# Kernel optimization log

Measured on AMD Instinct MI355X. Metric: run time of the kernel, lower is better.

Reference implementation:

```python
import jax, jax.numpy as jnp
import numpy as np

ALPHA = 0.2
NEG = -9e15
EPS = 1e-5


def _gat(h, adj, W, a, out_features):
    # h: [B,N,Fin], adj: [B,N,N], W: [Fin,Fout], a: [2*Fout,1]
    Wh = jnp.matmul(h, W)                      # [B,N,Fout]
    Wh1 = jnp.matmul(Wh, a[:out_features])     # [B,N,1]
    Wh2 = jnp.matmul(Wh, a[out_features:])     # [B,N,1]
    e = Wh1 + jnp.swapaxes(Wh2, 1, 2)          # [B,N,N]
    e = jax.nn.leaky_relu(e, negative_slope=ALPHA)
    scores = jnp.where(adj > 0, e, NEG)
    att = jax.nn.softmax(scores, axis=1)       # NOTE: dim=1 as in source
    return jnp.matmul(att, Wh)                 # [B,N,Fout]


def _layernorm(x, g, b):
    mu = jnp.mean(x, axis=-1, keepdims=True)
    var = jnp.var(x, axis=-1, keepdims=True)
    return (x - mu) * jax.lax.rsqrt(var + EPS) * g + b


def setup_inputs() -> dict:
    key = jax.random.key(0)
    ks = jax.random.split(key, 8)
    B, N, F, H = 2, 4096, 256, 1024
    x = jax.random.normal(ks[0], (B, N, F), dtype=jnp.float32)
    adj = jax.random.randint(ks[1], (B, N, N), 0, 2, dtype=jnp.int32)
    def xavier(k, shape):
        fan_in, fan_out = shape[0], shape[1]
        lim = np.sqrt(6.0 / (fan_in + fan_out))
        return jax.random.uniform(k, shape, jnp.float32, -lim, lim)
    return {
        "x": x,
        "adj": adj,
        "W1": xavier(ks[2], (F, F)),
        "a1": xavier(ks[3], (2 * F, 1)),
        "W2": xavier(ks[4], (F, F)),
        "a2": xavier(ks[5], (2 * F, 1)),
        "w_ff1": xavier(ks[6], (F, H)) ,
        "b_ff1": jnp.zeros((H,), jnp.float32),
        "w_ff2": xavier(ks[7], (H, F)),
        "b_ff2": jnp.zeros((F,), jnp.float32),
        "g_ln1": jnp.ones((F,), jnp.float32),
        "b_ln1": jnp.zeros((F,), jnp.float32),
        "g_ln2": jnp.ones((F,), jnp.float32),
        "b_ln2": jnp.zeros((F,), jnp.float32),
    }


def reference(x, adj, W1, a1, W2, a2, w_ff1, b_ff1, w_ff2, b_ff2,
              g_ln1, b_ln1, g_ln2, b_ln2):
    Fout = W1.shape[1]
    residual = x
    # dropout is a no-op in eval mode
    h = _gat(x, adj, W1, a1, Fout)          # single head -> cat is identity
    h = _gat(h, adj, W2, a2, W2.shape[1])
    h = _layernorm(residual + h, g_ln1, b_ln1)
    residual2 = h
    ff = jnp.matmul(jax.nn.relu(jnp.matmul(h, w_ff1) + b_ff1), w_ff2) + b_ff2
    return _layernorm(residual2 + ff, g_ln2, b_ln2)
```

## Files before the change

kernel.cpp:

```cpp
#include <hip/hip_runtime.h>
#include <math.h>

#define ALPHA 0.2f
#define NEGV  -9e15f
#define EPSV  1e-5f

constexpr int B_ = 2, N_ = 4096, F_ = 256, H_ = 1024;
constexpr int SPLIT_ = 16;
constexpr int SPLITJ_ = 4;

typedef __attribute__((ext_vector_type(4))) float f32x4;
typedef __attribute__((ext_vector_type(8))) short s16x8;

__device__ __forceinline__ unsigned short f2bf(float f) {
    unsigned u = __builtin_bit_cast(unsigned, f);
    u += 0x7fffu + ((u >> 16) & 1u);
    return (unsigned short)(u >> 16);
}

__global__ __launch_bounds__(256) void gemm2_kernel(
    const void* __restrict__ Ap, const unsigned short* __restrict__ Wt,
    const float* __restrict__ bias, void* __restrict__ Cp,
    unsigned short* __restrict__ Tout,
    int M, int Nc, int K, int relu, int a_bf16, int c_bf16)
{
    __shared__ unsigned short As[64 * 72];
    __shared__ unsigned short Bs[64 * 72];
    const int t = threadIdx.x;
    const int w = t >> 6, l = t & 63;
    const int quad = l >> 4, l15 = l & 15;
    const int iw = (w & 1) * 32, fw = (w >> 1) * 32;
    const int row0 = blockIdx.y * 64, col0 = blockIdx.x * 64;

    const int sr = t >> 2;
    const int sk = (t & 3) * 16;

    f32x4 acc[2][2];
    #pragma unroll
    for (int a = 0; a < 2; ++a)
        #pragma unroll
        for (int c = 0; c < 2; ++c) acc[a][c] = (f32x4)(0.f);

    for (int k0 = 0; k0 < K; k0 += 64) {
        if (a_bf16) {
            const unsigned short* ap =
                (const unsigned short*)Ap + (size_t)(row0 + sr) * K + k0 + sk;
            *(s16x8*)&As[sr * 72 + sk]     = *(const s16x8*)ap;
            *(s16x8*)&As[sr * 72 + sk + 8] = *(const s16x8*)(ap + 8);
        } else {
            const float* ap = (const float*)Ap + (size_t)(row0 + sr) * K + k0 + sk;
            #pragma unroll
            for (int u4 = 0; u4 < 4; ++u4) {
                const float4 v = *(const float4*)&ap[u4 * 4];
                ushort4 o;
                o.x = f2bf(v.x); o.y = f2bf(v.y); o.z = f2bf(v.z); o.w = f2bf(v.w);
                *(ushort4*)&As[sr * 72 + sk + u4 * 4] = o;
            }
        }
        {
            const unsigned short* bp = &Wt[(size_t)(col0 + sr) * K + k0 + sk];
            *(s16x8*)&Bs[sr * 72 + sk]     = *(const s16x8*)bp;
            *(s16x8*)&Bs[sr * 72 + sk + 8] = *(const s16x8*)(bp + 8);
        }
        __syncthreads();
        #pragma unroll
        for (int ks = 0; ks < 64; ks += 32) {
            s16x8 af[2], bf[2];
            #pragma unroll
            for (int it = 0; it < 2; ++it)
                af[it] = *(const s16x8*)&As[(iw + it * 16 + l15) * 72 + ks + quad * 8];
            #pragma unroll
            for (int ft = 0; ft < 2; ++ft)
                bf[ft] = *(const s16x8*)&Bs[(fw + ft * 16 + l15) * 72 + ks + quad * 8];
            #pragma unroll
            for (int it = 0; it < 2; ++it)
                #pragma unroll
                for (int ft = 0; ft < 2; ++ft)
                    acc[it][ft] = __builtin_amdgcn_mfma_f32_16x16x32_bf16(
                        af[it], bf[ft], acc[it][ft], 0, 0, 0);
        }
        __syncthreads();
    }

    #pragma unroll
    for (int ft = 0; ft < 2; ++ft) {
        const int col = col0 + fw + ft * 16 + l15;
        const float bv = bias ? bias[col] : 0.f;
        #pragma unroll
        for (int it = 0; it < 2; ++it) {
            float v0 = acc[it][ft][0] + bv, v1 = acc[it][ft][1] + bv;
            float v2 = acc[it][ft][2] + bv, v3 = acc[it][ft][3] + bv;
            if (relu) {
                v0 = fmaxf(v0, 0.f); v1 = fmaxf(v1, 0.f);
                v2 = fmaxf(v2, 0.f); v3 = fmaxf(v3, 0.f);
            }
            const int rbase = row0 + iw + it * 16 + quad * 4;
            if (c_bf16) {
                unsigned short* Cs = (unsigned short*)Cp;
                Cs[(size_t)(rbase + 0) * Nc + col] = f2bf(v0);
                Cs[(size_t)(rbase + 1) * Nc + col] = f2bf(v1);
                Cs[(size_t)(rbase + 2) * Nc + col] = f2bf(v2);
                Cs[(size_t)(rbase + 3) * Nc + col] = f2bf(v3);
            } else {
                float* Cf = (float*)Cp;
                Cf[(size_t)(rbase + 0) * Nc + col] = v0;
                Cf[(size_t)(rbase + 1) * Nc + col] = v1;
                Cf[(size_t)(rbase + 2) * Nc + col] = v2;
                Cf[(size_t)(rbase + 3) * Nc + col] = v3;
            }
            if (Tout) {
                const int bb = row0 >> 12;
                const int ibase = (row0 & (N_ - 1)) + iw + it * 16 + quad * 4;
                ushort4 o;
                o.x = f2bf(acc[it][ft][0]); o.y = f2bf(acc[it][ft][1]);
                o.z = f2bf(acc[it][ft][2]); o.w = f2bf(acc[it][ft][3]);
                *(ushort4*)&Tout[((size_t)bb * F_ + col) * N_ + ibase] = o;
            }
        }
    }
}

__global__ __launch_bounds__(256) void wh12_kernel(
    const float* __restrict__ Wh, const float* __restrict__ a,
    float* __restrict__ Wh1, float* __restrict__ Wh2)
{
    const int wid = threadIdx.x >> 6, lane = threadIdx.x & 63;
    const int row = blockIdx.x * 4 + wid;
    const float4 w  = *(const float4*)&Wh[(size_t)row * F_ + lane * 4];
    const float4 u1 = *(const float4*)&a[lane * 4];
    const float4 u2 = *(const float4*)&a[F_ + lane * 4];
    float s1 = w.x * u1.x + w.y * u1.y + w.z * u1.z + w.w * u1.w;
    float s2 = w.x * u2.x + w.y * u2.y + w.z * u2.z + w.w * u2.w;
    #pragma unroll
    for (int off = 32; off > 0; off >>= 1) {
        s1 += __shfl_down(s1, off);
        s2 += __shfl_down(s2, off);
    }
    if (lane == 0) { Wh1[row] = s1; Wh2[row] = s2; }
}

__global__ __launch_bounds__(256) void colstats_adj_kernel(
    const int* __restrict__ adj, unsigned long long* __restrict__ maskOut,
    const float* __restrict__ Wh1, const float* __restrict__ Wh2,
    float* __restrict__ pM, float* __restrict__ pS)
{
    const int t = threadIdx.x;
    const int j = blockIdx.x * 256 + t;
    const int sp = blockIdx.y;
    const int b = blockIdx.z;
    const int i0 = sp * (N_ / SPLIT_);
    const int w = t >> 6, l = t & 63;
    const float w2 = Wh2[b * N_ + j];
    const float* __restrict__ w1p = Wh1 + b * N_ + i0;
    const int* __restrict__ ap = adj + ((size_t)b * N_ + i0) * N_ + j;

    float m = -3.4e38f, s = 0.f;
    for (int c = 0; c < N_ / SPLIT_; c += 8) {
        int v[8];
        #pragma unroll
        for (int u = 0; u < 8; ++u) v[u] = ap[(size_t)(c + u) * N_];
        float x[8];
        #pragma unroll
        for (int u = 0; u < 8; ++u) {
            const bool act = v[u] > 0;
            const unsigned long long bm = __ballot(act);
            if (l == 0)
                maskOut[((size_t)b * N_ + i0 + c + u) * (N_ / 64) + blockIdx.x * 4 + w] = bm;
            const float e0 = w1p[c + u] + w2;
            const float e = fmaxf(e0, ALPHA * e0);
            x[u] = act ? e : NEGV;
        }
        const float cm = fmaxf(fmaxf(fmaxf(x[0], x[1]), fmaxf(x[2], x[3])),
                               fmaxf(fmaxf(x[4], x[5]), fmaxf(x[6], x[7])));
        const float nm = fmaxf(m, cm);
        float cs = 0.f;
        #pragma unroll
        for (int u = 0; u < 8; ++u) cs += __expf(x[u] - nm);
        s = s * __expf(m - nm) + cs;
        m = nm;
    }
    pM[((size_t)b * SPLIT_ + sp) * N_ + j] = m;
    pS[((size_t)b * SPLIT_ + sp) * N_ + j] = s;
}

__global__ __launch_bounds__(256) void colstats3_kernel(
    const unsigned long long* __restrict__ mask,
    const float* __restrict__ Wh1, const float* __restrict__ Wh2,
    float* __restrict__ pM, float* __restrict__ pS)
{
    const int t = threadIdx.x;
    const int j = blockIdx.x * 256 + t;
    const int sp = blockIdx.y;
    const int b = blockIdx.z;
    const int i0 = sp * (N_ / SPLIT_);
    const int w = t >> 6;
    const int jbit = t & 63;
    const float w2 = Wh2[b * N_ + j];
    const unsigned long long* __restrict__ mbase =
        mask + ((size_t)b * N_ + i0) * (N_ / 64) + blockIdx.x * 4 + w;
    const float* __restrict__ w1p = Wh1 + b * N_ + i0;

    float m = -3.4e38f, s = 0.f;
    for (int c = 0; c < N_ / SPLIT_; c += 8) {
        float x[8];
        #pragma unroll
        for (int u = 0; u < 8; ++u) {
            const unsigned long long mw = mbase[(size_t)(c + u) * (N_ / 64)];
            const float e0 = w1p[c + u] + w2;
            const float e = fmaxf(e0, ALPHA * e0);
            x[u] = ((mw >> jbit) & 1ull) ? e : NEGV;
        }
        const float cm = fmaxf(fmaxf(fmaxf(x[0], x[1]), fmaxf(x[2], x[3])),
                               fmaxf(fmaxf(x[4], x[5]), fmaxf(x[6], x[7])));
        const float nm = fmaxf(m, cm);
        float cs = 0.f;
        #pragma unroll
        for (int u = 0; u < 8; ++u) cs += __expf(x[u] - nm);
        s = s * __expf(m - nm) + cs;
        m = nm;
    }
    pM[((size_t)b * SPLIT_ + sp) * N_ + j] = m;
    pS[((size_t)b * SPLIT_ + sp) * N_ + j] = s;
}

__global__ __launch_bounds__(256) void colfin2_kernel(
    const float* __restrict__ pM, const float* __restrict__ pS,
    float* __restrict__ Mo)
{
    const int j = blockIdx.x * 256 + threadIdx.x;
    const int b = blockIdx.y;
    float m = -3.4e38f;
    #pragma unroll
    for (int s = 0; s < SPLIT_; ++s)
        m = fmaxf(m, pM[((size_t)b * SPLIT_ + s) * N_ + j]);
    float sum = 0.f;
    #pragma unroll
    for (int s = 0; s < SPLIT_; ++s)
        sum += pS[((size_t)b * SPLIT_ + s) * N_ + j] *
               __expf(pM[((size_t)b * SPLIT_ + s) * N_ + j] - m);
    Mo[b * N_ + j] = m + logf(sum);
}

__global__ __launch_bounds__(256) void transp_kernel(
    const float* __restrict__ src, unsigned short* __restrict__ dst, int R, int Cc)
{
    __shared__ float T[64][65];
    const int t = threadIdx.x;
    const int r0 = blockIdx.x * 64, c0 = blockIdx.y * 64;
    #pragma unroll
    for (int s = 0; s < 4; ++s) {
        const int rr = s * 16 + (t >> 4);
        const int cq = t & 15;
        const float4 v = *(const float4*)&src[(size_t)(r0 + rr) * Cc + c0 + cq * 4];
        T[rr][cq * 4 + 0] = v.x; T[rr][cq * 4 + 1] = v.y;
        T[rr][cq * 4 + 2] = v.z; T[rr][cq * 4 + 3] = v.w;
    }
    __syncthreads();
    #pragma unroll
    for (int s = 0; s < 4; ++s) {
        const int cr = s * 16 + (t >> 4);
        const int rq = t & 15;
        ushort4 o;
        o.x = f2bf(T[rq * 4 + 0][cr]);
        o.y = f2bf(T[rq * 4 + 1][cr]);
        o.z = f2bf(T[rq * 4 + 2][cr]);
        o.w = f2bf(T[rq * 4 + 3][cr]);
        *(ushort4*)&dst[(size_t)(c0 + cr) * R + r0 + rq * 4] = o;
    }
}

__global__ __launch_bounds__(256) void att_mfma3_kernel(
    const unsigned short* __restrict__ mask16, const unsigned short* __restrict__ Wht,
    const float* __restrict__ Wh1, const float* __restrict__ Wh2,
    const float* __restrict__ Mo, float* __restrict__ part)
{
    __shared__ unsigned short Bs[256 * 72];
    __shared__ unsigned short Ps[64 * 72];
    __shared__ float w2s[1024];
    __shared__ float mos[1024];

    const int t = threadIdx.x;
    const int w = t >> 6, l = t & 63;
    const int quad = l >> 4, l15 = l & 15;
    const int b = blockIdx.z;
    const int i0 = blockIdx.x * 64;
    const int sp = blockIdx.y;
    const int jbase = sp * (N_ / SPLITJ_);

    const int pi = t >> 2;
    const int pj4 = t & 3;
    const float w1i = Wh1[b * N_ + i0 + pi];
    const unsigned short* __restrict__ mrow =
        mask16 + ((size_t)b * N_ + i0 + pi) * (N_ / 16);
    const unsigned short* __restrict__ WhtB = Wht + (size_t)b * F_ * N_;

    {
        const float4 a = *(const float4*)&Wh2[b * N_ + jbase + t * 4];
        const float4 c = *(const float4*)&Mo[b * N_ + jbase + t * 4];
        *(float4*)&w2s[t * 4] = a;
        *(float4*)&mos[t * 4] = c;
    }

    f32x4 acc[4][4];
    #pragma unroll
    for (int it = 0; it < 4; ++it)
        #pragma unroll
        for (int ft = 0; ft < 4; ++ft) acc[it][ft] = (f32x4)(0.f);

    const int f0s = t >> 3;
    const int prt = (t & 7) * 8;
    s16x8 breg[8];
    {
        const int jb = jbase;
        #pragma unroll
        for (int s = 0; s < 8; ++s)
            breg[s] = *(const s16x8*)&WhtB[(size_t)(f0s + s * 32) * N_ + jb + prt];
    }
    unsigned short mb_cur = mrow[jbase / 16 + pj4];
    __syncthreads();

    constexpr int NITER = (N_ / SPLITJ_) / 64;
    for (int itr = 0; itr < NITER; ++itr) {
        const int jb = jbase + itr * 64;
        #pragma unroll
        for (int s = 0; s < 8; ++s)
            *(s16x8*)&Bs[(f0s + s * 32) * 72 + prt] = breg[s];
        {
            const unsigned mb = mb_cur;
            const int jl = itr * 64 + pj4 * 16;
            #pragma unroll
            for (int u4 = 0; u4 < 4; ++u4) {
                const float4 w2v = *(const float4*)&w2s[jl + u4 * 4];
                const float4 mov = *(const float4*)&mos[jl + u4 * 4];
                ushort4 o;
                unsigned short* op = &o.x;
                #pragma unroll
                for (int u = 0; u < 4; ++u) {
                    const float xw = w1i + (&w2v.x)[u];
                    const float e = fmaxf(xw, ALPHA * xw);
                    const float x2 = ((mb >> (u4 * 4 + u)) & 1u) ? e : NEGV;
                    op[u] = f2bf(__expf(x2 - (&mov.x)[u]));
                }
                *(ushort4*)&Ps[pi * 72 + pj4 * 16 + u4 * 4] = o;
            }
        }
        __syncthreads();
        if (itr + 1 < NITER) {
            const int jn = jb + 64;
            #pragma unroll
            for (int s = 0; s < 8; ++s)
                breg[s] = *(const s16x8*)&WhtB[(size_t)(f0s + s * 32) * N_ + jn + prt];
            mb_cur = mrow[jn / 16 + pj4];
        }
        #pragma unroll
        for (int ks = 0; ks < 64; ks += 32) {
            s16x8 af[4];
            #pragma unroll
            for (int it = 0; it < 4; ++it)
                af[it] = *(const s16x8*)&Ps[(it * 16 + l15) * 72 + ks + quad * 8];
            #pragma unroll
            for (int ft = 0; ft < 4; ++ft) {
                const s16x8 bf =
                    *(const s16x8*)&Bs[(w * 64 + ft * 16 + l15) * 72 + ks + quad * 8];
                #pragma unroll
                for (int it = 0; it < 4; ++it)
                    acc[it][ft] = __builtin_amdgcn_mfma_f32_16x16x32_bf16(
                        af[it], bf, acc[it][ft], 0, 0, 0);
            }
        }
        __syncthreads();
    }

    float* __restrict__ pout = part + ((size_t)sp * B_ + b) * N_ * F_;
    #pragma unroll
    for (int it = 0; it < 4; ++it)
        #pragma unroll
        for (int ft = 0; ft < 4; ++ft) {
            const int col = w * 64 + ft * 16 + l15;
            #pragma unroll
            for (int rr = 0; rr < 4; ++rr) {
                const int row = i0 + it * 16 + quad * 4 + rr;
                pout[(size_t)row * F_ + col] = acc[it][ft][rr];
            }
        }
}

__global__ __launch_bounds__(256) void reduce4_kernel(
    const float* __restrict__ p, float* __restrict__ out)
{
    const size_t i = ((size_t)blockIdx.x * 256 + threadIdx.x) * 4;
    const size_t S = (size_t)B_ * N_ * F_;
    const float4 a = *(const float4*)&p[i];
    const float4 b = *(const float4*)&p[i + S];
    const float4 c = *(const float4*)&p[i + 2 * S];
    const float4 d = *(const float4*)&p[i + 3 * S];
    float4 o;
    o.x = a.x + b.x + c.x + d.x;
    o.y = a.y + b.y + c.y + d.y;
    o.z = a.z + b.z + c.z + d.z;
    o.w = a.w + b.w + c.w + d.w;
    *(float4*)&out[i] = o;
}

__global__ __launch_bounds__(256) void addln_kernel(
    const float* __restrict__ X, const float* __restrict__ Y,
    const float* __restrict__ g, const float* __restrict__ bta,
    float* __restrict__ out)
{
    const int row = blockIdx.x;
    const int t = threadIdx.x;
    const size_t idx = (size_t)row * F_ + t;
    const float v = X[idx] + Y[idx];
    float s1 = v, s2 = v * v;
    #pragma unroll
    for (int off = 32; off > 0; off >>= 1) {
        s1 += __shfl_down(s1, off);
        s2 += __shfl_down(s2, off);
    }
    __shared__ float r1[4], r2[4];
    __shared__ float mu_s, rs_s;
    const int wid = t >> 6, lane = t & 63;
    if (lane == 0) { r1[wid] = s1; r2[wid] = s2; }
    __syncthreads();
    if (t == 0) {
        const float a = r1[0] + r1[1] + r1[2] + r1[3];
        const float q = r2[0] + r2[1] + r2[2] + r2[3];
        const float mu = a * (1.f / F_);
        const float var = q * (1.f / F_) - mu * mu;
        mu_s = mu;
        rs_s = rsqrtf(var + EPSV);
    }
    __syncthreads();
    out[idx] = (v - mu_s) * rs_s * g[t] + bta[t];
}

extern "C" void kernel_launch(void* const* d_in, const int* in_sizes, int n_in,
                              void* d_out, int out_size, void* d_ws, size_t ws_size,
                              hipStream_t stream)
{
    const float* x     = (const float*)d_in[0];
    const int*   adj   = (const int*)d_in[1];
    const float* W1    = (const float*)d_in[2];
    const float* a1    = (const float*)d_in[3];
    const float* W2    = (const float*)d_in[4];
    const float* a2    = (const float*)d_in[5];
    const float* w_ff1 = (const float*)d_in[6];
    const float* b_ff1 = (const float*)d_in[7];
    const float* w_ff2 = (const float*)d_in[8];
    const float* b_ff2 = (const float*)d_in[9];
    const float* g_ln1 = (const float*)d_in[10];
    const float* b_ln1 = (const float*)d_in[11];
    const float* g_ln2 = (const float*)d_in[12];
    const float* b_ln2 = (const float*)d_in[13];
    float* out = (float*)d_out;

    const int Rtot = B_ * N_;
    float* ws = (float*)d_ws;
    float* Wh_buf = ws;
    float* g1out  = ws + 2097152;
    float* ln1    = ws + 4194304;
    float* part   = ws + 6291456;
    unsigned short* mid_us = (unsigned short*)(ws + 14680064);
    unsigned short* Wht    = (unsigned short*)(ws + 18874368);
    unsigned long long* mask = (unsigned long long*)(ws + 19922944);
    unsigned short* mask16 = (unsigned short*)mask;
    float* Wh1v = ws + 20971520;
    float* Wh2v = Wh1v + 8192;
    float* Mo   = Wh2v + 8192;
    float* pM   = Mo + 8192;
    float* pS   = pM + (size_t)B_ * SPLIT_ * N_;
    unsigned short* Wt = (unsigned short*)(ws + 21299200);

    const dim3 statsG(N_ / 256, SPLIT_, B_);
    const dim3 finG(N_ / 256, B_);
    const dim3 attG(N_ / 64, SPLITJ_, B_);

    transp_kernel<<<dim3(4, 4), 256, 0, stream>>>(W1, Wt, 256, 256);
    gemm2_kernel<<<dim3(F_ / 64, Rtot / 64), 256, 0, stream>>>(
        x, Wt, nullptr, Wh_buf, Wht, Rtot, F_, F_, 0, 0, 0);
    wh12_kernel<<<Rtot / 4, 256, 0, stream>>>(Wh_buf, a1, Wh1v, Wh2v);
    colstats_adj_kernel<<<statsG, 256, 0, stream>>>(adj, mask, Wh1v, Wh2v, pM, pS);
    colfin2_kernel<<<finG, 256, 0, stream>>>(pM, pS, Mo);
    att_mfma3_kernel<<<attG, 256, 0, stream>>>(mask16, Wht, Wh1v, Wh2v, Mo, part);
    reduce4_kernel<<<2048, 256, 0, stream>>>(part, g1out);

    transp_kernel<<<dim3(4, 4), 256, 0, stream>>>(W2, Wt, 256, 256);
    gemm2_kernel<<<dim3(F_ / 64, Rtot / 64), 256, 0, stream>>>(
        g1out, Wt, nullptr, Wh_buf, Wht, Rtot, F_, F_, 0, 0, 0);
    wh12_kernel<<<Rtot / 4, 256, 0, stream>>>(Wh_buf, a2, Wh1v, Wh2v);
    colstats3_kernel<<<statsG, 256, 0, stream>>>(mask, Wh1v, Wh2v, pM, pS);
    colfin2_kernel<<<finG, 256, 0, stream>>>(pM, pS, Mo);
    att_mfma3_kernel<<<attG, 256, 0, stream>>>(mask16, Wht, Wh1v, Wh2v, Mo, part);
    reduce4_kernel<<<2048, 256, 0, stream>>>(part, g1out);

    addln_kernel<<<Rtot, 256, 0, stream>>>(x, g1out, g_ln1, b_ln1, ln1);

    transp_kernel<<<dim3(4, 16), 256, 0, stream>>>(w_ff1, Wt, 256, 1024);
    gemm2_kernel<<<dim3(H_ / 64, Rtot / 64), 256, 0, stream>>>(
        ln1, Wt, b_ff1, mid_us, nullptr, Rtot, H_, F_, 1, 0, 1);
    transp_kernel<<<dim3(16, 4), 256, 0, stream>>>(w_ff2, Wt, 1024, 256);
    gemm2_kernel<<<dim3(F_ / 64, Rtot / 64), 256, 0, stream>>>(
        mid_us, Wt, b_ff2, out, nullptr, Rtot, F_, H_, 0, 1, 0);

    addln_kernel<<<Rtot, 256, 0, stream>>>(ln1, out, g_ln2, b_ln2, out);
}
```

Baseline: 424.0 us.

## Fuse attention projections into 128-tile GEMM, merge transposes, fold reduce into layernorm

```diff
diff --git a/kernel.cpp b/kernel.cpp
--- a/kernel.cpp
+++ b/kernel.cpp
@@ -18,99 +18,146 @@
     return (unsigned short)(u >> 16);
 }
 
-__global__ __launch_bounds__(256) void gemm2_kernel(
+__global__ __launch_bounds__(256) void zero_kernel(float* __restrict__ p)
+{
+    const int i = (blockIdx.x * 256 + threadIdx.x) * 4;
+    *(float4*)&p[i] = make_float4(0.f, 0.f, 0.f, 0.f);
+}
+
+__global__ __launch_bounds__(256) void transp_all_kernel(
+    const float* __restrict__ W1, const float* __restrict__ W2,
+    const float* __restrict__ F1s, const float* __restrict__ F2s,
+    unsigned short* __restrict__ D1, unsigned short* __restrict__ D2,
+    unsigned short* __restrict__ D3, unsigned short* __restrict__ D4)
+{
+    const int mi = blockIdx.z;
+    const float* src; unsigned short* dst; int R, Cc;
+    if (mi == 0)      { src = W1;  dst = D1; R = 256;  Cc = 256; }
+    else if (mi == 1) { src = W2;  dst = D2; R = 256;  Cc = 256; }
+    else if (mi == 2) { src = F1s; dst = D3; R = 256;  Cc = 1024; }
+    else              { src = F2s; dst = D4; R = 1024; Cc = 256; }
+    const int r0 = blockIdx.x * 64, c0 = blockIdx.y * 64;
+    if (r0 >= R || c0 >= Cc) return;
+
+    __shared__ float T[64][65];
+    const int t = threadIdx.x;
+    #pragma unroll
+    for (int s = 0; s < 4; ++s) {
+        const int rr = s * 16 + (t >> 4);
+        const int cq = t & 15;
+        const float4 v = *(const float4*)&src[(size_t)(r0 + rr) * Cc + c0 + cq * 4];
+        T[rr][cq * 4 + 0] = v.x; T[rr][cq * 4 + 1] = v.y;
+        T[rr][cq * 4 + 2] = v.z; T[rr][cq * 4 + 3] = v.w;
+    }
+    __syncthreads();
+    #pragma unroll
+    for (int s = 0; s < 4; ++s) {
+        const int cr = s * 16 + (t >> 4);
+        const int rq = t & 15;
+        ushort4 o;
+        o.x = f2bf(T[rq * 4 + 0][cr]);
+        o.y = f2bf(T[rq * 4 + 1][cr]);
+        o.z = f2bf(T[rq * 4 + 2][cr]);
+        o.w = f2bf(T[rq * 4 + 3][cr]);
+        *(ushort4*)&dst[(size_t)(c0 + cr) * R + r0 + rq * 4] = o;
+    }
+}
+
+__global__ __launch_bounds__(256) void gemm128_kernel(
     const void* __restrict__ Ap, const unsigned short* __restrict__ Wt,
     const float* __restrict__ bias, void* __restrict__ Cp,
-    unsigned short* __restrict__ Tout,
-    int M, int Nc, int K, int relu, int a_bf16, int c_bf16)
-{
-    __shared__ unsigned short As[64 * 72];
-    __shared__ unsigned short Bs[64 * 72];
+    unsigned short* __restrict__ Tout, const float* __restrict__ wha,
+    float* __restrict__ Wh1, float* __restrict__ Wh2,
+    int Nc, int K, int relu, int a_bf16, int c_mode)
+{
+    __shared__ unsigned short As[128 * 72];
+    __shared__ unsigned short Bs[128 * 72];
     const int t = threadIdx.x;
     const int w = t >> 6, l = t & 63;
     const int quad = l >> 4, l15 = l & 15;
-    const int iw = (w & 1) * 32, fw = (w >> 1) * 32;
-    const int row0 = blockIdx.y * 64, col0 = blockIdx.x * 64;
-
-    const int sr = t >> 2;
-    const int sk = (t & 3) * 16;
-
-    f32x4 acc[2][2];
-    #pragma unroll
-    for (int a = 0; a < 2; ++a)
-        #pragma unroll
-        for (int c = 0; c < 2; ++c) acc[a][c] = (f32x4)(0.f);
+    const int wr = w & 1, wc = w >> 1;
+    const int row0 = blockIdx.y * 128, col0 = blockIdx.x * 128;
+    const int sr = t >> 1;
+    const int sk = (t & 1) * 32;
+
+    f32x4 acc[4][4];
+    #pragma unroll
+    for (int it = 0; it < 4; ++it)
+        #pragma unroll
+        for (int ft = 0; ft < 4; ++ft) acc[it][ft] = (f32x4)(0.f);
 
     for (int k0 = 0; k0 < K; k0 += 64) {
         if (a_bf16) {
             const unsigned short* ap =
                 (const unsigned short*)Ap + (size_t)(row0 + sr) * K + k0 + sk;
-            *(s16x8*)&As[sr * 72 + sk]     = *(const s16x8*)ap;
-            *(s16x8*)&As[sr * 72 + sk + 8] = *(const s16x8*)(ap + 8);
+            #pragma unroll
+            for (int u = 0; u < 4; ++u)
+                *(s16x8*)&As[sr * 72 + sk + u * 8] = *(const s16x8*)(ap + u * 8);
         } else {
             const float* ap = (const float*)Ap + (size_t)(row0 + sr) * K + k0 + sk;
             #pragma unroll
-            for (int u4 = 0; u4 < 4; ++u4) {
-                const float4 v = *(const float4*)&ap[u4 * 4];
+            for (int u = 0; u < 8; ++u) {
+                const float4 v = *(const float4*)(ap + u * 4);
                 ushort4 o;
                 o.x = f2bf(v.x); o.y = f2bf(v.y); o.z = f2bf(v.z); o.w = f2bf(v.w);
-                *(ushort4*)&As[sr * 72 + sk + u4 * 4] = o;
+                *(ushort4*)&As[sr * 72 + sk + u * 4] = o;
             }
         }
         {
-            const unsigned short* bp = &Wt[(size_t)(col0 + sr) * K + k0 + sk];
-            *(s16x8*)&Bs[sr * 72 + sk]     = *(const s16x8*)bp;
-            *(s16x8*)&Bs[sr * 72 + sk + 8] = *(const s16x8*)(bp + 8);
+            const unsigned short* bp = Wt + (size_t)(col0 + sr) * K + k0 + sk;
+            #pragma unroll
+            for (int u = 0; u < 4; ++u)
+                *(s16x8*)&Bs[sr * 72 + sk + u * 8] = *(const s16x8*)(bp + u * 8);
         }
         __syncthreads();
         #pragma unroll
         for (int ks = 0; ks < 64; ks += 32) {
-            s16x8 af[2], bf[2];
-            #pragma unroll
-            for (int it = 0; it < 2; ++it)
-                af[it] = *(const s16x8*)&As[(iw + it * 16 + l15) * 72 + ks + quad * 8];
-            #pragma unroll
-            for (int ft = 0; ft < 2; ++ft)
-                bf[ft] = *(const s16x8*)&Bs[(fw + ft * 16 + l15) * 72 + ks + quad * 8];
-            #pragma unroll
-            for (int it = 0; it < 2; ++it)
+            s16x8 af[4], bf[4];
+            #pragma unroll
+            for (int it = 0; it < 4; ++it)
+                af[it] = *(const s16x8*)&As[(wr * 64 + it * 16 + l15) * 72 + ks + quad * 8];
+            #pragma unroll
+            for (int ft = 0; ft < 4; ++ft)
+                bf[ft] = *(const s16x8*)&Bs[(wc * 64 + ft * 16 + l15) * 72 + ks + quad * 8];
+            #pragma unroll
+            for (int ft = 0; ft < 4; ++ft)
                 #pragma unroll
-                for (int ft = 0; ft < 2; ++ft)
+                for (int it = 0; it < 4; ++it)
                     acc[it][ft] = __builtin_amdgcn_mfma_f32_16x16x32_bf16(
                         af[it], bf[ft], acc[it][ft], 0, 0, 0);
         }
         __syncthreads();
     }
 
-    #pragma unroll
-    for (int ft = 0; ft < 2; ++ft) {
-        const int col = col0 + fw + ft * 16 + l15;
-        const float bv = bias ? bias[col] : 0.f;
-        #pragma unroll
-        for (int it = 0; it < 2; ++it) {
-            float v0 = acc[it][ft][0] + bv, v1 = acc[it][ft][1] + bv;
-            float v2 = acc[it][ft][2] + bv, v3 = acc[it][ft][3] + bv;
-            if (relu) {
-                v0 = fmaxf(v0, 0.f); v1 = fmaxf(v1, 0.f);
-                v2 = fmaxf(v2, 0.f); v3 = fmaxf(v3, 0.f);
-            }
-            const int rbase = row0 + iw + it * 16 + quad * 4;
-            if (c_bf16) {
-                unsigned short* Cs = (unsigned short*)Cp;
-                Cs[(size_t)(rbase + 0) * Nc + col] = f2bf(v0);
-                Cs[(size_t)(rbase + 1) * Nc + col] = f2bf(v1);
-                Cs[(size_t)(rbase + 2) * Nc + col] = f2bf(v2);
-                Cs[(size_t)(rbase + 3) * Nc + col] = f2bf(v3);
-            } else {
-                float* Cf = (float*)Cp;
-                Cf[(size_t)(rbase + 0) * Nc + col] = v0;
-                Cf[(size_t)(rbase + 1) * Nc + col] = v1;
-                Cf[(size_t)(rbase + 2) * Nc + col] = v2;
-                Cf[(size_t)(rbase + 3) * Nc + col] = v3;
-            }
-            if (Tout) {
-                const int bb = row0 >> 12;
-                const int ibase = (row0 & (N_ - 1)) + iw + it * 16 + quad * 4;
+    if (c_mode) {
+        #pragma unroll
+        for (int ft = 0; ft < 4; ++ft) {
+            const int col = col0 + wc * 64 + ft * 16 + l15;
+            const float bv = bias ? bias[col] : 0.f;
+            #pragma unroll
+            for (int it = 0; it < 4; ++it) {
+                const int rbase = row0 + wr * 64 + it * 16 + quad * 4;
+                #pragma unroll
+                for (int rr = 0; rr < 4; ++rr) {
+                    float v = acc[it][ft][rr] + bv;
+                    if (relu) v = fmaxf(v, 0.f);
+                    if (c_mode == 2)
+                        ((unsigned short*)Cp)[(size_t)(rbase + rr) * Nc + col] = f2bf(v);
+                    else
+                        ((float*)Cp)[(size_t)(rbase + rr) * Nc + col] = v;
+                }
+            }
+        }
+    }
+
+    if (Tout) {
+        const int bb = row0 >> 12;
+        #pragma unroll
+        for (int ft = 0; ft < 4; ++ft) {
+            const int col = col0 + wc * 64 + ft * 16 + l15;
+            #pragma unroll
+            for (int it = 0; it < 4; ++it) {
+                const int ibase = (row0 & (N_ - 1)) + wr * 64 + it * 16 + quad * 4;
                 ushort4 o;
                 o.x = f2bf(acc[it][ft][0]); o.y = f2bf(acc[it][ft][1]);
                 o.z = f2bf(acc[it][ft][2]); o.w = f2bf(acc[it][ft][3]);
@@ -118,25 +165,37 @@
             }
         }
     }
-}
-
-__global__ __launch_bounds__(256) void wh12_kernel(
-    const float* __restrict__ Wh, const float* __restrict__ a,
-    float* __restrict__ Wh1, float* __restrict__ Wh2)
-{
-    const int wid = threadIdx.x >> 6, lane = threadIdx.x & 63;
-    const int row = blockIdx.x * 4 + wid;
-    const float4 w  = *(const float4*)&Wh[(size_t)row * F_ + lane * 4];
-    const float4 u1 = *(const float4*)&a[lane * 4];
-    const float4 u2 = *(const float4*)&a[F_ + lane * 4];
-    float s1 = w.x * u1.x + w.y * u1.y + w.z * u1.z + w.w * u1.w;
-    float s2 = w.x * u2.x + w.y * u2.y + w.z * u2.z + w.w * u2.w;
-    #pragma unroll
-    for (int off = 32; off > 0; off >>= 1) {
-        s1 += __shfl_down(s1, off);
-        s2 += __shfl_down(s2, off);
-    }
-    if (lane == 0) { Wh1[row] = s1; Wh2[row] = s2; }
+
+    if (wha) {
+        float a1v[4], a2v[4];
+        #pragma unroll
+        for (int ft = 0; ft < 4; ++ft) {
+            const int col = col0 + wc * 64 + ft * 16 + l15;
+            a1v[ft] = wha[col];
+            a2v[ft] = wha[F_ + col];
+        }
+        #pragma unroll
+        for (int it = 0; it < 4; ++it)
+            #pragma unroll
+            for (int rr = 0; rr < 4; ++rr) {
+                float s1 = 0.f, s2 = 0.f;
+                #pragma unroll
+                for (int ft = 0; ft < 4; ++ft) {
+                    s1 += acc[it][ft][rr] * a1v[ft];
+                    s2 += acc[it][ft][rr] * a2v[ft];
+                }
+                #pragma unroll
+                for (int mkk = 1; mkk < 16; mkk <<= 1) {
+                    s1 += __shfl_xor(s1, mkk);
+                    s2 += __shfl_xor(s2, mkk);
+                }
+                if (l15 == 0) {
+                    const int row = row0 + wr * 64 + it * 16 + quad * 4 + rr;
+                    atomicAdd(&Wh1[row], s1);
+                    atomicAdd(&Wh2[row], s2);
+                }
+            }
+    }
 }
 
 __global__ __launch_bounds__(256) void colstats_adj_kernel(
@@ -239,34 +298,6 @@
         sum += pS[((size_t)b * SPLIT_ + s) * N_ + j] *
                __expf(pM[((size_t)b * SPLIT_ + s) * N_ + j] - m);
     Mo[b * N_ + j] = m + logf(sum);
-}
-
-__global__ __launch_bounds__(256) void transp_kernel(
-    const float* __restrict__ src, unsigned short* __restrict__ dst, int R, int Cc)
-{
-    __shared__ float T[64][65];
-    const int t = threadIdx.x;
-    const int r0 = blockIdx.x * 64, c0 = blockIdx.y * 64;
-    #pragma unroll
-    for (int s = 0; s < 4; ++s) {
-        const int rr = s * 16 + (t >> 4);
-        const int cq = t & 15;
-        const float4 v = *(const float4*)&src[(size_t)(r0 + rr) * Cc + c0 + cq * 4];
-        T[rr][cq * 4 + 0] = v.x; T[rr][cq * 4 + 1] = v.y;
-        T[rr][cq * 4 + 2] = v.z; T[rr][cq * 4 + 3] = v.w;
-    }
-    __syncthreads();
-    #pragma unroll
-    for (int s = 0; s < 4; ++s) {
-        const int cr = s * 16 + (t >> 4);
-        const int rq = t & 15;
-        ushort4 o;
-        o.x = f2bf(T[rq * 4 + 0][cr]);
-        o.y = f2bf(T[rq * 4 + 1][cr]);
-        o.z = f2bf(T[rq * 4 + 2][cr]);
-        o.w = f2bf(T[rq * 4 + 3][cr]);
-        *(ushort4*)&dst[(size_t)(c0 + cr) * R + r0 + rq * 4] = o;
-    }
 }
 
 __global__ __launch_bounds__(256) void att_mfma3_kernel(
@@ -385,8 +416,8 @@
         }
 }
 
-__global__ __launch_bounds__(256) void reduce4_kernel(
-    const float* __restrict__ p, float* __restrict__ out)
+__global__ __launch_bounds__(256) void reduce4b_kernel(
+    const float* __restrict__ p, unsigned short* __restrict__ outb)
 {
     const size_t i = ((size_t)blockIdx.x * 256 + threadIdx.x) * 4;
     const size_t S = (size_t)B_ * N_ * F_;
@@ -394,12 +425,47 @@
     const float4 b = *(const float4*)&p[i + S];
     const float4 c = *(const float4*)&p[i + 2 * S];
     const float4 d = *(const float4*)&p[i + 3 * S];
-    float4 o;
-    o.x = a.x + b.x + c.x + d.x;
-    o.y = a.y + b.y + c.y + d.y;
-    o.z = a.z + b.z + c.z + d.z;
-    o.w = a.w + b.w + c.w + d.w;
-    *(float4*)&out[i] = o;
+    ushort4 o;
+    o.x = f2bf(a.x + b.x + c.x + d.x);
+    o.y = f2bf(a.y + b.y + c.y + d.y);
+    o.z = f2bf(a.z + b.z + c.z + d.z);
+    o.w = f2bf(a.w + b.w + c.w + d.w);
+    *(ushort4*)&outb[i] = o;
+}
+
+__global__ __launch_bounds__(256) void addln4_kernel(
+    const float* __restrict__ X, const float* __restrict__ p,
+    const float* __restrict__ g, const float* __restrict__ bta,
+    float* __restrict__ outf, unsigned short* __restrict__ outb)
+{
+    const int row = blockIdx.x;
+    const int t = threadIdx.x;
+    const size_t idx = (size_t)row * F_ + t;
+    const size_t S = (size_t)B_ * N_ * F_;
+    const float v = X[idx] + p[idx] + p[idx + S] + p[idx + 2 * S] + p[idx + 3 * S];
+    float s1 = v, s2 = v * v;
+    #pragma unroll
+    for (int off = 32; off > 0; off >>= 1) {
+        s1 += __shfl_down(s1, off);
+        s2 += __shfl_down(s2, off);
+    }
+    __shared__ float r1[4], r2[4];
+    __shared__ float mu_s, rs_s;
+    const int wid = t >> 6, lane = t & 63;
+    if (lane == 0) { r1[wid] = s1; r2[wid] = s2; }
+    __syncthreads();
+    if (t == 0) {
+        const float a = r1[0] + r1[1] + r1[2] + r1[3];
+        const float q = r2[0] + r2[1] + r2[2] + r2[3];
+        const float mu = a * (1.f / F_);
+        const float var = q * (1.f / F_) - mu * mu;
+        mu_s = mu;
+        rs_s = rsqrtf(var + EPSV);
+    }
+    __syncthreads();
+    const float r = (v - mu_s) * rs_s * g[t] + bta[t];
+    outf[idx] = r;
+    outb[idx] = f2bf(r);
 }
 
 __global__ __launch_bounds__(256) void addln_kernel(
@@ -455,52 +521,55 @@
     float* out = (float*)d_out;
 
     const int Rtot = B_ * N_;
-    float* ws = (float*)d_ws;
-    float* Wh_buf = ws;
-    float* g1out  = ws + 2097152;
-    float* ln1    = ws + 4194304;
-    float* part   = ws + 6291456;
-    unsigned short* mid_us = (unsigned short*)(ws + 14680064);
-    unsigned short* Wht    = (unsigned short*)(ws + 18874368);
-    unsigned long long* mask = (unsigned long long*)(ws + 19922944);
+    char* wsb = (char*)d_ws;
+    float* part  = (float*)wsb;
+    float* ln1   = (float*)(wsb + 33554432);
+    float* ffout = (float*)(wsb + 41943040);
+    unsigned short* mid  = (unsigned short*)(wsb + 50331648);
+    unsigned short* ln1b = (unsigned short*)(wsb + 67108864);
+    unsigned short* g1b  = (unsigned short*)(wsb + 71303168);
+    unsigned short* Wht  = (unsigned short*)(wsb + 75497472);
+    unsigned long long* mask = (unsigned long long*)(wsb + 79691776);
     unsigned short* mask16 = (unsigned short*)mask;
-    float* Wh1v = ws + 20971520;
-    float* Wh2v = Wh1v + 8192;
-    float* Mo   = Wh2v + 8192;
-    float* pM   = Mo + 8192;
-    float* pS   = pM + (size_t)B_ * SPLIT_ * N_;
-    unsigned short* Wt = (unsigned short*)(ws + 21299200);
+    unsigned short* Wt1  = (unsigned short*)(wsb + 83886080);
+    unsigned short* Wt2  = Wt1 + 65536;
+    unsigned short* Wtf1 = Wt2 + 65536;
+    unsigned short* Wtf2 = Wtf1 + 262144;
+    float* WhA1 = (float*)(wsb + 85196800);
+    float* WhA2 = WhA1 + 8192;
+    float* WhB1 = WhA2 + 8192;
+    float* WhB2 = WhB1 + 8192;
+    float* Mo   = (float*)(wsb + 85327872);
+    float* pM   = (float*)(wsb + 85360640);
+    float* pS   = (float*)(wsb + 85884928);
 
     const dim3 statsG(N_ / 256, SPLIT_, B_);
     const dim3 finG(N_ / 256, B_);
     const dim3 attG(N_ / 64, SPLITJ_, B_);
 
-    transp_kernel<<<dim3(4, 4), 256, 0, stream>>>(W1, Wt, 256, 256);
-    gemm2_kernel<<<dim3(F_ / 64, Rtot / 64), 256, 0, stream>>>(
-        x, Wt, nullptr, Wh_buf, Wht, Rtot, F_, F_, 0, 0, 0);
-    wh12_kernel<<<Rtot / 4, 256, 0, stream>>>(Wh_buf, a1, Wh1v, Wh2v);
-    colstats_adj_kernel<<<statsG, 256, 0, stream>>>(adj, mask, Wh1v, Wh2v, pM, pS);
+    zero_kernel<<<32, 256, 0, stream>>>(WhA1);
+    transp_all_kernel<<<dim3(16, 16, 4), 256, 0, stream>>>(
+        W1, W2, w_ff1, w_ff2, Wt1, Wt2, Wtf1, Wtf2);
+
+    gemm128_kernel<<<dim3(2, 64), 256, 0, stream>>>(
+        x, Wt1, nullptr, nullptr, Wht, a1, WhA1, WhA2, F_, F_, 0, 0, 0);
+    colstats_adj_kernel<<<statsG, 256, 0, stream>>>(adj, mask, WhA1, WhA2, pM, pS);
     colfin2_kernel<<<finG, 256, 0, stream>>>(pM, pS, Mo);
-    att_mfma3_kernel<<<attG, 256, 0, stream>>>(mask16, Wht, Wh1v, Wh2v, Mo, part);
-    reduce4_kernel<<<2048, 256, 0, stream>>>(part, g1out);
-
-    transp_kernel<<<dim3(4, 4), 256, 0, stream>>>(W2, Wt, 256, 256);
-    gemm2_kernel<<<dim3(F_ / 64, Rtot / 64), 256, 0, stream>>>(
-        g1out, Wt, nullptr, Wh_buf, Wht, Rtot, F_, F_, 0, 0, 0);
-    wh12_kernel<<<Rtot / 4, 256, 0, stream>>>(Wh_buf, a2, Wh1v, Wh2v);
-    colstats3_kernel<<<statsG, 256, 0, stream>>>(mask, Wh1v, Wh2v, pM, pS);
+    att_mfma3_kernel<<<attG, 256, 0, stream>>>(mask16, Wht, WhA1, WhA2, Mo, part);
+    reduce4b_kernel<<<2048, 256, 0, stream>>>(part, g1b);
+
+    gemm128_kernel<<<dim3(2, 64), 256, 0, stream>>>(
+        g1b, Wt2, nullptr, nullptr, Wht, a2, WhB1, WhB2, F_, F_, 0, 1, 0);
+    colstats3_kernel<<<statsG, 256, 0, stream>>>(mask, WhB1, WhB2, pM, pS);
     colfin2_kernel<<<finG, 256, 0, stream>>>(pM, pS, Mo);
-    att_mfma3_kernel<<<attG, 256, 0, stream>>>(mask16, Wht, Wh1v, Wh2v, Mo, part);
-    reduce4_kernel<<<2048, 256, 0, stream>>>(part, g1out);
-
-    addln_kernel<<<Rtot, 256, 0, stream>>>(x, g1out, g_ln1, b_ln1, ln1);
-
-    transp_kernel<<<dim3(4, 16), 256, 0, stream>>>(w_ff1, Wt, 256, 1024);
-    gemm2_kernel<<<dim3(H_ / 64, Rtot / 64), 256, 0, stream>>>(
-        ln1, Wt, b_ff1, mid_us, nullptr, Rtot, H_, F_, 1, 0, 1);
-    transp_kernel<<<dim3(16, 4), 256, 0, stream>>>(w_ff2, Wt, 1024, 256);
-    gemm2_kernel<<<dim3(F_ / 64, Rtot / 64), 256, 0, stream>>>(
-        mid_us, Wt, b_ff2, out, nullptr, Rtot, F_, H_, 0, 1, 0);
-
-    addln_kernel<<<Rtot, 256, 0, stream>>>(ln1, out, g_ln2, b_ln2, out);
-}
+    att_mfma3_kernel<<<attG, 256, 0, stream>>>(mask16, Wht, WhB1, WhB2, Mo, part);
+
+    addln4_kernel<<<Rtot, 256, 0, stream>>>(x, part, g_ln1, b_ln1, ln1, ln1b);
+
+    gemm128_kernel<<<dim3(8, 64), 256, 0, stream>>>(
+        ln1b, Wtf1, b_ff1, mid, nullptr, nullptr, nullptr, nullptr, H_, F_, 1, 1, 2);
+    gemm128_kernel<<<dim3(2, 64), 256, 0, stream>>>(
+        mid, Wtf2, b_ff2, ffout, nullptr, nullptr, nullptr, nullptr, F_, H_, 0, 1, 1);
+
+    addln_kernel<<<Rtot, 256, 0, stream>>>(ln1, ffout, g_ln2, b_ln2, out);
+}
```

Result: no change. 423.6 us (-0.1%).
